# Optimization experiments

Hardware: AMD Instinct MI355X
Metric: run time of the kernel (lower is better)

## Reference

```python
import jax, jax.numpy as jnp
import numpy as np

N = 100000   # nodes
E = 3200000  # directed edges
EPS = 1e-5   # batchnorm eps


def setup_inputs() -> dict:
    key = jax.random.key(0)
    ks = jax.random.split(key, 12)
    x = jax.random.normal(ks[0], (N, 128), jnp.float32)
    edge_index = jax.random.randint(ks[1], (2, E), 0, N, dtype=jnp.int32).astype(jnp.int64)
    W1 = jax.random.normal(ks[2], (128, 256), jnp.float32) * (1.0 / np.sqrt(128))
    W2 = jax.random.normal(ks[3], (256, 256), jnp.float32) * (1.0 / np.sqrt(256))
    W3 = jax.random.normal(ks[4], (256, 40), jnp.float32) * (1.0 / np.sqrt(256))
    return {
        "x": x, "edge_index": edge_index,
        "W1": W1, "b1": jnp.zeros((256,), jnp.float32),
        "W2": W2, "b2": jnp.zeros((256,), jnp.float32),
        "W3": W3, "b3": jnp.zeros((40,), jnp.float32),
        "g1": jnp.ones((256,), jnp.float32), "be1": jnp.zeros((256,), jnp.float32),
        "g2": jnp.ones((256,), jnp.float32), "be2": jnp.zeros((256,), jnp.float32),
    }


def _gcn_conv(x, src, dst, norm, W, b):
    # GCNConv: transform then normalized sparse aggregation (A_hat @ (x W)) + b
    h = x @ W                              # [N, F_out]
    msg = h[src] * norm[:, None]           # gather + edge scaling, [E+N, F_out]
    return jax.ops.segment_sum(msg, dst, num_segments=N) + b


def _bn(h, g, b):
    # BatchNorm over the node dimension (batch stats, biased variance)
    m = h.mean(axis=0)
    v = h.var(axis=0)
    return (h - m) * jax.lax.rsqrt(v + EPS) * g + b


def reference(x, edge_index, W1, b1, W2, b2, W3, b3, g1, be1, g2, be2):
    # add self-loops (A + I), symmetric degree normalization D^-1/2 (A+I) D^-1/2
    loop = jnp.arange(N, dtype=edge_index.dtype)
    src = jnp.concatenate([edge_index[0], loop])
    dst = jnp.concatenate([edge_index[1], loop])
    deg = jax.ops.segment_sum(jnp.ones_like(src, jnp.float32), dst, num_segments=N)
    dinv = jax.lax.rsqrt(jnp.maximum(deg, 1.0))
    norm = dinv[src] * dinv[dst]           # [E+N]

    h = _gcn_conv(x, src, dst, norm, W1, b1)
    h = jax.nn.relu(_bn(h, g1, be1))       # dropout: identity (eval mode)
    h = _gcn_conv(h, src, dst, norm, W2, b2)
    h = jax.nn.relu(_bn(h, g2, be2))
    h = _gcn_conv(h, src, dst, norm, W3, b3)
    return jax.nn.log_softmax(h, axis=1)
```

## Files before the change

### kernel.cpp

```cpp
#include <hip/hip_runtime.h>
#include <hip/hip_bf16.h>
#include <math.h>

#define NNODES 100000
#define NEDGES 3200000
#define BN_EPS 1e-5f
#define NCH 391

typedef unsigned int uint;
typedef unsigned short ushort;
typedef __attribute__((ext_vector_type(8))) short bf16x8;
typedef __attribute__((ext_vector_type(4))) float f32x4;

__device__ inline float bflo(uint u) { return __uint_as_float(u << 16); }
__device__ inline float bfhi(uint u) { return __uint_as_float(u & 0xffff0000u); }
__device__ inline ushort f2bf(float f) {
    __hip_bfloat16 h = __float2bfloat16(f);
    union { __hip_bfloat16 b; ushort u; } c; c.b = h; return c.u;
}


__global__ void k_setup(const int* __restrict__ edst, int* __restrict__ cnt,
                        const float* __restrict__ x, ushort* __restrict__ xbf16,
                        const float* __restrict__ W1, const float* __restrict__ W2,
                        const float* __restrict__ W3, ushort* __restrict__ W1t,
                        ushort* __restrict__ W2t, ushort* __restrict__ W3t) {
    int b = blockIdx.x;
    if (b < 6250) {
        int e = (b * 256 + threadIdx.x) * 2;
        int2 v = *(const int2*)(edst + e);
        atomicAdd(&cnt[v.x], 1);
        atomicAdd(&cnt[v.y], 1);
    } else if (b < 18750) {
        int i = (b - 6250) * 256 + threadIdx.x;
        float4 v = ((const float4*)x)[i];
        ushort4 o; o.x=f2bf(v.x); o.y=f2bf(v.y); o.z=f2bf(v.z); o.w=f2bf(v.w);
        ((ushort4*)xbf16)[i] = o;
    } else {
        int bb = b - 18750;
        if (bb < 256) {
            for (int k = threadIdx.x; k < 128; k += 256)
                W1t[bb * 128 + k] = f2bf(W1[(size_t)k * 256 + bb]);
        } else if (bb < 512) {
            int n = bb - 256;
            for (int k = threadIdx.x; k < 256; k += 256)
                W2t[n * 256 + k] = f2bf(W2[(size_t)k * 256 + n]);
        } else {
            int n = bb - 512;
            for (int k = threadIdx.x; k < 256; k += 256)
                W3t[n * 256 + k] = (n < 40) ? f2bf(W3[(size_t)k * 40 + n]) : (ushort)0;
        }
    }
}

__global__ void k_deg(const int* __restrict__ cnt, float* __restrict__ dinv,
                      int* __restrict__ chunksums) {
    __shared__ int s[256];
    int i = blockIdx.x * 256 + threadIdx.x;
    int c = (i < NNODES) ? cnt[i] : 0;
    if (i < NNODES) dinv[i] = rsqrtf((float)c + 1.0f);
    s[threadIdx.x] = c;
    __syncthreads();
    for (int o = 128; o > 0; o >>= 1) {
        if (threadIdx.x < o) s[threadIdx.x] += s[threadIdx.x + o];
        __syncthreads();
    }
    if (threadIdx.x == 0) chunksums[blockIdx.x] = s[0];
}

__global__ void k_scan1(int* __restrict__ chunksums, int* __restrict__ rowstart) {
    __shared__ int s[512];
    int t = threadIdx.x;
    int v = (t < NCH) ? chunksums[t] : 0;
    s[t] = v;
    __syncthreads();
    for (int o = 1; o < 512; o <<= 1) {
        int add = (t >= o) ? s[t - o] : 0;
        __syncthreads();
        s[t] += add;
        __syncthreads();
    }
    if (t < NCH) chunksums[t] = s[t] - v;
    if (t == NCH - 1) rowstart[NNODES] = s[t];
}

__global__ void k_scan2(const int* __restrict__ cnt, const int* __restrict__ chunkbase,
                        int* __restrict__ rowstart, int* __restrict__ cursor) {
    __shared__ int s[256];
    int t = threadIdx.x;
    int i = blockIdx.x * 256 + t;
    int v = (i < NNODES) ? cnt[i] : 0;
    s[t] = v;
    __syncthreads();
    for (int o = 1; o < 256; o <<= 1) {
        int add = (t >= o) ? s[t - o] : 0;
        __syncthreads();
        s[t] += add;
        __syncthreads();
    }
    if (i < NNODES) {
        int excl = s[t] - v + chunkbase[blockIdx.x];
        rowstart[i] = excl;
        cursor[i]   = excl;
    }
}

__global__ void k_scatter(const int* __restrict__ src, const int* __restrict__ dst,
                          const float* __restrict__ dinv, int* __restrict__ cursor,
                          int2* __restrict__ pairs) {
    int e = blockIdx.x * 256 + threadIdx.x;
    if (e >= NEDGES) return;
    int s = src[e], d = dst[e];
    int p = atomicAdd(&cursor[d], 1);
    float w = dinv[s] * dinv[d];
    pairs[p] = make_int2(s, __float_as_int(w));
}


template <int F, int U>
__global__ __launch_bounds__(256) void k_aggh(
    const ushort* __restrict__ X, ushort* __restrict__ Y,
    const int2* __restrict__ pairs, const int* __restrict__ rowstart,
    const float* __restrict__ dinv) {
    constexpr int CPL = F / 32;
    const int wv = threadIdx.x >> 6;
    const int lane = threadIdx.x & 63;
    const int h = lane >> 5, l32 = lane & 31;
    const int d = blockIdx.x * 4 + wv;
    const int r0 = rowstart[d], r1 = rowstart[d + 1];
    const ushort* Xb = X + (size_t)CPL * l32;
    float acc[CPL] = {};
    int p = r0;
    for (; p + 2 * U <= r1; p += 2 * U) {
        int2 e[U];
#pragma unroll
        for (int j = 0; j < U; ++j) e[j] = pairs[p + 2 * j + h];
        if constexpr (CPL == 8) {
            uint4 u[U];
#pragma unroll
            for (int j = 0; j < U; ++j) u[j] = *(const uint4*)(Xb + (size_t)e[j].x * F);
#pragma unroll
            for (int j = 0; j < U; ++j) {
                float w = __int_as_float(e[j].y);
                acc[0]=fmaf(w,bflo(u[j].x),acc[0]); acc[1]=fmaf(w,bfhi(u[j].x),acc[1]);
                acc[2]=fmaf(w,bflo(u[j].y),acc[2]); acc[3]=fmaf(w,bfhi(u[j].y),acc[3]);
                acc[4]=fmaf(w,bflo(u[j].z),acc[4]); acc[5]=fmaf(w,bfhi(u[j].z),acc[5]);
                acc[6]=fmaf(w,bflo(u[j].w),acc[6]); acc[7]=fmaf(w,bfhi(u[j].w),acc[7]);
            }
        } else {
            uint2 u[U];
#pragma unroll
            for (int j = 0; j < U; ++j) u[j] = *(const uint2*)(Xb + (size_t)e[j].x * F);
#pragma unroll
            for (int j = 0; j < U; ++j) {
                float w = __int_as_float(e[j].y);
                acc[0]=fmaf(w,bflo(u[j].x),acc[0]); acc[1]=fmaf(w,bfhi(u[j].x),acc[1]);
                acc[2]=fmaf(w,bflo(u[j].y),acc[2]); acc[3]=fmaf(w,bfhi(u[j].y),acc[3]);
            }
        }
    }
    for (; p + 2 <= r1; p += 2) {
        int2 e = pairs[p + h];
        float w = __int_as_float(e.y);
        if constexpr (CPL == 8) {
            uint4 u = *(const uint4*)(Xb + (size_t)e.x * F);
            acc[0]=fmaf(w,bflo(u.x),acc[0]); acc[1]=fmaf(w,bfhi(u.x),acc[1]);
            acc[2]=fmaf(w,bflo(u.y),acc[2]); acc[3]=fmaf(w,bfhi(u.y),acc[3]);
            acc[4]=fmaf(w,bflo(u.z),acc[4]); acc[5]=fmaf(w,bfhi(u.z),acc[5]);
            acc[6]=fmaf(w,bflo(u.w),acc[6]); acc[7]=fmaf(w,bfhi(u.w),acc[7]);
        } else {
            uint2 u = *(const uint2*)(Xb + (size_t)e.x * F);
            acc[0]=fmaf(w,bflo(u.x),acc[0]); acc[1]=fmaf(w,bfhi(u.x),acc[1]);
            acc[2]=fmaf(w,bflo(u.y),acc[2]); acc[3]=fmaf(w,bfhi(u.y),acc[3]);
        }
    }
    if (p < r1 && h == 0) {
        int2 e = pairs[p];
        float w = __int_as_float(e.y);
        if constexpr (CPL == 8) {
            uint4 u = *(const uint4*)(Xb + (size_t)e.x * F);
            acc[0]=fmaf(w,bflo(u.x),acc[0]); acc[1]=fmaf(w,bfhi(u.x),acc[1]);
            acc[2]=fmaf(w,bflo(u.y),acc[2]); acc[3]=fmaf(w,bfhi(u.y),acc[3]);
            acc[4]=fmaf(w,bflo(u.z),acc[4]); acc[5]=fmaf(w,bfhi(u.z),acc[5]);
            acc[6]=fmaf(w,bflo(u.w),acc[6]); acc[7]=fmaf(w,bfhi(u.w),acc[7]);
        } else {
            uint2 u = *(const uint2*)(Xb + (size_t)e.x * F);
            acc[0]=fmaf(w,bflo(u.x),acc[0]); acc[1]=fmaf(w,bfhi(u.x),acc[1]);
            acc[2]=fmaf(w,bflo(u.y),acc[2]); acc[3]=fmaf(w,bfhi(u.y),acc[3]);
        }
    }
#pragma unroll
    for (int c = 0; c < CPL; ++c) acc[c] += __shfl_xor(acc[c], 32);
    if (h == 0) {
        float di = dinv[d], ws = di * di;
        if constexpr (CPL == 8) {
            uint4 u = *(const uint4*)(Xb + (size_t)d * F);
            acc[0]=fmaf(ws,bflo(u.x),acc[0]); acc[1]=fmaf(ws,bfhi(u.x),acc[1]);
            acc[2]=fmaf(ws,bflo(u.y),acc[2]); acc[3]=fmaf(ws,bfhi(u.y),acc[3]);
            acc[4]=fmaf(ws,bflo(u.z),acc[4]); acc[5]=fmaf(ws,bfhi(u.z),acc[5]);
            acc[6]=fmaf(ws,bflo(u.w),acc[6]); acc[7]=fmaf(ws,bfhi(u.w),acc[7]);
            uint4 o;
            o.x = (uint)f2bf(acc[0]) | ((uint)f2bf(acc[1]) << 16);
            o.y = (uint)f2bf(acc[2]) | ((uint)f2bf(acc[3]) << 16);
            o.z = (uint)f2bf(acc[4]) | ((uint)f2bf(acc[5]) << 16);
            o.w = (uint)f2bf(acc[6]) | ((uint)f2bf(acc[7]) << 16);
            *(uint4*)(Y + (size_t)d * F + CPL * l32) = o;
        } else {
            uint2 u = *(const uint2*)(Xb + (size_t)d * F);
            acc[0]=fmaf(ws,bflo(u.x),acc[0]); acc[1]=fmaf(ws,bfhi(u.x),acc[1]);
            acc[2]=fmaf(ws,bflo(u.y),acc[2]); acc[3]=fmaf(ws,bfhi(u.y),acc[3]);
            uint2 o;
            o.x = (uint)f2bf(acc[0]) | ((uint)f2bf(acc[1]) << 16);
            o.y = (uint)f2bf(acc[2]) | ((uint)f2bf(acc[3]) << 16);
            *(uint2*)(Y + (size_t)d * F + CPL * l32) = o;
        }
    }
}


__global__ __launch_bounds__(256) void k_agg40lsm(
    const ushort* __restrict__ X, float* __restrict__ out,
    const int2* __restrict__ pairs, const int* __restrict__ rowstart,
    const float* __restrict__ dinv, const float* __restrict__ bias) {
    int t = threadIdx.x;
    int wid = t >> 6, lane = t & 63;
    int sub = lane >> 5, l32 = lane & 31;
    int d = blockIdx.x * 8 + wid * 2 + sub;
    bool act = l32 < 20;
    int col = act ? 2 * l32 : 0;
    const int r0 = rowstart[d], r1 = rowstart[d + 1];
    float a0 = 0.f, a1 = 0.f;
    int p = r0;
    for (; p + 8 <= r1; p += 8) {
        int2 e[8]; uint u[8];
#pragma unroll
        for (int j = 0; j < 8; ++j) e[j] = pairs[p + j];
#pragma unroll
        for (int j = 0; j < 8; ++j) u[j] = *(const uint*)(X + (size_t)e[j].x * 40 + col);
#pragma unroll
        for (int j = 0; j < 8; ++j) {
            float w = __int_as_float(e[j].y);
            a0 = fmaf(w, bflo(u[j]), a0); a1 = fmaf(w, bfhi(u[j]), a1);
        }
    }
    for (; p < r1; ++p) {
        int2 e = pairs[p];
        uint u = *(const uint*)(X + (size_t)e.x * 40 + col);
        float w_ = __int_as_float(e.y);
        a0 = fmaf(w_, bflo(u), a0); a1 = fmaf(w_, bfhi(u), a1);
    }
    float di = dinv[d], ws = di * di;
    uint us = *(const uint*)(X + (size_t)d * 40 + col);
    a0 = fmaf(ws, bflo(us), a0); a1 = fmaf(ws, bfhi(us), a1);
    if (act) { a0 += bias[col]; a1 += bias[col + 1]; }
    else     { a0 = -INFINITY;  a1 = -INFINITY; }
    float mx = fmaxf(a0, a1);
    for (int o = 16; o > 0; o >>= 1) mx = fmaxf(mx, __shfl_xor(mx, o, 32));
    float e = act ? (expf(a0 - mx) + expf(a1 - mx)) : 0.f;
    float s = e;
    for (int o = 16; o > 0; o >>= 1) s += __shfl_xor(s, o, 32);
    float ls = logf(s);
    if (act)
        *(float2*)(out + (size_t)d * 40 + col) = make_float2(a0 - mx - ls, a1 - mx - ls);
}


__device__ inline bf16x8 bnrelu8(bf16x8 v, const float* scsh, int ch) {
    bf16x8 r;
#pragma unroll
    for (int j = 0; j < 8; ++j) {
        float f = __uint_as_float(((uint)(ushort)v[j]) << 16);
        f = fmaxf(fmaf(f, scsh[ch + j], scsh[256 + ch + j]), 0.f);
        r[j] = (short)f2bf(f);
    }
    return r;
}

template <int K, bool BNA, bool STATS>
__global__ __launch_bounds__(256) void k_gmm(
    const ushort* __restrict__ A, const ushort* __restrict__ Bt,
    const float* __restrict__ bsums, const float* __restrict__ g,
    const float* __restrict__ be, ushort* __restrict__ C,
    float* __restrict__ sums_out) {
    __shared__ ushort As[128 * 32];
    __shared__ ushort Bs[128 * 32];
    __shared__ float scsh[512];
    if constexpr (BNA) {
        int c = threadIdx.x;
        float mean = bsums[c] * (1.0f / NNODES);
        float var  = bsums[256 + c] * (1.0f / NNODES) - mean * mean;
        float sc = g[c] * rsqrtf(var + BN_EPS);
        scsh[c] = sc;
        scsh[256 + c] = be[c] - mean * sc;
        __syncthreads();
    }
    const int m0 = blockIdx.x * 128;
    const int n0 = blockIdx.y * 128;
    const int tid = threadIdx.x;
    const int lane = tid & 63;
    const int wid = tid >> 6;
    const int wr = wid >> 1, wc = wid & 1;
    const int sr1 = tid >> 2, sc_ = tid & 3;
    const int sr2 = sr1 + 64;
    const int ssl1 = sr1 * 32 + ((sc_ ^ ((sr1 >> 1) & 3)) * 8);
    const int ssl2 = sr2 * 32 + ((sc_ ^ ((sr2 >> 1) & 3)) * 8);
    const size_t ga1 = (size_t)min(m0 + sr1, NNODES - 1) * K + sc_ * 8;
    const size_t ga2 = (size_t)min(m0 + sr2, NNODES - 1) * K + sc_ * 8;
    const size_t gb1 = (size_t)(n0 + sr1) * K + sc_ * 8;
    const size_t gb2 = (size_t)(n0 + sr2) * K + sc_ * 8;
    const int kc = lane >> 4, rr = lane & 15;
    f32x4 acc[4][4] = {};
    for (int k0 = 0; k0 < K; k0 += 32) {
        bf16x8 av1 = *(const bf16x8*)(A + ga1 + k0);
        bf16x8 av2 = *(const bf16x8*)(A + ga2 + k0);
        bf16x8 bv1 = *(const bf16x8*)(Bt + gb1 + k0);
        bf16x8 bv2 = *(const bf16x8*)(Bt + gb2 + k0);
        if constexpr (BNA) {
            int ch = k0 + sc_ * 8;
            av1 = bnrelu8(av1, scsh, ch);
            av2 = bnrelu8(av2, scsh, ch);
        }
        if (k0) __syncthreads();
        *(bf16x8*)(As + ssl1) = av1;
        *(bf16x8*)(As + ssl2) = av2;
        *(bf16x8*)(Bs + ssl1) = bv1;
        *(bf16x8*)(Bs + ssl2) = bv2;
        __syncthreads();
        bf16x8 af[4], bfr[4];
#pragma unroll
        for (int f = 0; f < 4; ++f) {
            int ar = wr * 64 + f * 16 + rr;
            int br = wc * 64 + f * 16 + rr;
            af[f]  = *(const bf16x8*)(As + ar * 32 + ((kc ^ ((ar >> 1) & 3)) * 8));
            bfr[f] = *(const bf16x8*)(Bs + br * 32 + ((kc ^ ((br >> 1) & 3)) * 8));
        }
#pragma unroll
        for (int fm = 0; fm < 4; ++fm)
#pragma unroll
            for (int fn = 0; fn < 4; ++fn)
                acc[fm][fn] = __builtin_amdgcn_mfma_f32_16x16x32_bf16(af[fm], bfr[fn], acc[fm][fn], 0, 0, 0);
    }
    const int crow0 = m0 + wr * 64 + (lane >> 4) * 4;
    const int ccol0 = n0 + wc * 64 + (lane & 15);
#pragma unroll
    for (int fm = 0; fm < 4; ++fm) {
#pragma unroll
        for (int r = 0; r < 4; ++r) {
            int m = crow0 + fm * 16 + r;
            if (m >= NNODES) continue;
#pragma unroll
            for (int fn = 0; fn < 4; ++fn)
                C[(size_t)m * 256 + ccol0 + fn * 16] = f2bf(acc[fm][fn][r]);
        }
    }
    if constexpr (STATS) {
#pragma unroll
        for (int fn = 0; fn < 4; ++fn) {
            float s = 0.f, s2 = 0.f;
#pragma unroll
            for (int fm = 0; fm < 4; ++fm)
#pragma unroll
                for (int r = 0; r < 4; ++r) {
                    int m = crow0 + fm * 16 + r;
                    if (m < NNODES) { float v = acc[fm][fn][r]; s += v; s2 += v * v; }
                }
            s  += __shfl_xor(s, 16);  s  += __shfl_xor(s, 32);
            s2 += __shfl_xor(s2, 16); s2 += __shfl_xor(s2, 32);
            if (lane < 16) {
                int ch = ccol0 + fn * 16;
                atomicAdd(&sums_out[ch], s);
                atomicAdd(&sums_out[256 + ch], s2);
            }
        }
    }
}


__global__ __launch_bounds__(256) void k_gmm3m(
    const ushort* __restrict__ A, const ushort* __restrict__ Bt,
    const float* __restrict__ bsums, const float* __restrict__ g,
    const float* __restrict__ be, ushort* __restrict__ C) {
    __shared__ ushort As[128 * 64];
    __shared__ ushort Bs[48 * 64];
    __shared__ float scsh[512];
    {
        int c = threadIdx.x;
        float mean = bsums[c] * (1.0f / NNODES);
        float var  = bsums[256 + c] * (1.0f / NNODES) - mean * mean;
        float sc = g[c] * rsqrtf(var + BN_EPS);
        scsh[c] = sc;
        scsh[256 + c] = be[c] - mean * sc;
        __syncthreads();
    }
    const int m0 = blockIdx.x * 128;
    const int tid = threadIdx.x;
    const int lane = tid & 63;
    const int wm = tid >> 6;
    const int kc = lane >> 4, rr = lane & 15;
    f32x4 acc[2][3] = {};
    for (int k0 = 0; k0 < 256; k0 += 64) {
        bf16x8 avs[4];
        int arow[4], ach[4];
#pragma unroll
        for (int i = 0; i < 4; ++i) {
            int c = i * 256 + tid;
            arow[i] = c >> 3; ach[i] = c & 7;
            int m = min(m0 + arow[i], NNODES - 1);
            bf16x8 v = *(const bf16x8*)(A + (size_t)m * 256 + k0 + ach[i] * 8);
            avs[i] = bnrelu8(v, scsh, k0 + ach[i] * 8);
        }
        bf16x8 bvs[2];
#pragma unroll
        for (int i = 0; i < 2; ++i) {
            int c = i * 256 + tid;
            if (c < 384) {
                int row = c >> 3, ch = c & 7;
                bvs[i] = *(const bf16x8*)(Bt + (size_t)row * 256 + k0 + ch * 8);
            }
        }
        if (k0) __syncthreads();
#pragma unroll
        for (int i = 0; i < 4; ++i)
            *(bf16x8*)(As + arow[i] * 64 + ((ach[i] ^ (arow[i] & 7)) * 8)) = avs[i];
#pragma unroll
        for (int i = 0; i < 2; ++i) {
            int c = i * 256 + tid;
            if (c < 384) {
                int row = c >> 3, ch = c & 7;
                *(bf16x8*)(Bs + row * 64 + ((ch ^ (row & 7)) * 8)) = bvs[i];
            }
        }
        __syncthreads();
#pragma unroll
        for (int ks = 0; ks < 2; ++ks) {
            bf16x8 af[2], bfm[3];
#pragma unroll
            for (int fm = 0; fm < 2; ++fm) {
                int ar = wm * 32 + fm * 16 + rr;
                af[fm] = *(const bf16x8*)(As + ar * 64 + (((ks * 4 + kc) ^ (ar & 7)) * 8));
            }
#pragma unroll
            for (int fn = 0; fn < 3; ++fn) {
                int br = fn * 16 + rr;
                bfm[fn] = *(const bf16x8*)(Bs + br * 64 + (((ks * 4 + kc) ^ (br & 7)) * 8));
            }
#pragma unroll
            for (int fm = 0; fm < 2; ++fm)
#pragma unroll
                for (int fn = 0; fn < 3; ++fn)
                    acc[fm][fn] = __builtin_amdgcn_mfma_f32_16x16x32_bf16(af[fm], bfm[fn], acc[fm][fn], 0, 0, 0);
        }
    }
    const int crow0 = m0 + wm * 32 + (lane >> 4) * 4;
    const int ccol = lane & 15;
#pragma unroll
    for (int fm = 0; fm < 2; ++fm)
#pragma unroll
        for (int r = 0; r < 4; ++r) {
            int m = crow0 + fm * 16 + r;
            if (m >= NNODES) continue;
#pragma unroll
            for (int fn = 0; fn < 3; ++fn) {
                int col = fn * 16 + ccol;
                if (col < 40) C[(size_t)m * 40 + col] = f2bf(acc[fm][fn][r]);
            }
        }
}


__global__ void k_bnstats_bf(const uint* __restrict__ H, float* __restrict__ sums) {
    int t = threadIdx.x;
    int pp = t & 127, half = t >> 7;
    size_t row0 = (size_t)blockIdx.x * 256 + half * 128;
    float s0=0, s20=0, s1=0, s21=0;
    for (int i = 0; i < 128; ++i) {
        size_t m = row0 + i;
        if (m >= NNODES) break;
        uint u = H[m * 128 + pp];
        float v0 = bflo(u), v1 = bfhi(u);
        s0 += v0; s20 += v0*v0; s1 += v1; s21 += v1*v1;
    }
    atomicAdd(&sums[2*pp],       s0);
    atomicAdd(&sums[2*pp+1],     s1);
    atomicAdd(&sums[256+2*pp],   s20);
    atomicAdd(&sums[256+2*pp+1], s21);
}


extern "C" void kernel_launch(void* const* d_in, const int* in_sizes, int n_in,
                              void* d_out, int out_size, void* d_ws, size_t ws_size,
                              hipStream_t stream) {
    const float* x  = (const float*)d_in[0];
    const int*   ei = (const int*)d_in[1];
    const float* W1 = (const float*)d_in[2];
    const float* W2 = (const float*)d_in[4];
    const float* W3 = (const float*)d_in[6];
    const float* b3 = (const float*)d_in[7];
    const float* g1 = (const float*)d_in[8];
    const float* be1 = (const float*)d_in[9];
    const float* g2 = (const float*)d_in[10];
    const float* be2 = (const float*)d_in[11];
    float* out = (float*)d_out;

    const int* esrc = ei;
    const int* edst = ei + NEDGES;

    char* p = (char*)d_ws;
    auto alloc = [&](size_t bytes) { char* r = p; p += (bytes + 511) & ~(size_t)511; return r; };
    float* dinv     = (float*)alloc((size_t)NNODES * 4);
    int*   cnt      = (int*)  alloc((size_t)NNODES * 4);
    int*   rowstart = (int*)  alloc((size_t)(NNODES + 1) * 4);
    int*   cursor   = (int*)  alloc((size_t)NNODES * 4);
    int*   chunksums= (int*)  alloc((size_t)NCH * 4);
    float* stats    = (float*)alloc((size_t)2048 * 4);
    ushort* W1t     = (ushort*)alloc((size_t)256 * 128 * 2);
    ushort* W2t     = (ushort*)alloc((size_t)256 * 256 * 2);
    ushort* W3t     = (ushort*)alloc((size_t)48 * 256 * 2);
    int2*  pairs    = (int2*) alloc((size_t)NEDGES * 8);
    char*  R1       = alloc((size_t)NNODES * 256 * 2);
    char*  R2       = alloc((size_t)NNODES * 256 * 2);
    char*  R3       = alloc((size_t)NNODES * 256 * 2);

    ushort* xbf16 = (ushort*)R1;
    ushort* P_bf  = (ushort*)R1 + (size_t)NNODES * 128;
    ushort* t3_bf = (ushort*)R1;
    ushort* h1_bf = (ushort*)R2;
    ushort* h2_bf = (ushort*)R2;
    ushort* t_bf  = (ushort*)R3;

    float* sums1 = stats;
    float* sums2 = stats + 1024;

    hipMemsetAsync(cnt, 0, (size_t)NNODES * 4, stream);
    hipMemsetAsync(stats, 0, (size_t)2048 * 4, stream);

    k_setup<<<19310, 256, 0, stream>>>(edst, cnt, x, xbf16, W1, W2, W3, W1t, W2t, W3t);
    k_deg<<<NCH, 256, 0, stream>>>(cnt, dinv, chunksums);
    k_scan1<<<1, 512, 0, stream>>>(chunksums, rowstart);
    k_scan2<<<NCH, 256, 0, stream>>>(cnt, chunksums, rowstart, cursor);
    k_scatter<<<NEDGES / 256, 256, 0, stream>>>(esrc, edst, dinv, cursor, pairs);

    dim3 ggrid((NNODES + 127) / 128, 2);

    k_aggh<128, 8><<<NNODES / 4, 256, 0, stream>>>(xbf16, P_bf, pairs, rowstart, dinv);
    k_gmm<128, false, true><<<ggrid, 256, 0, stream>>>(P_bf, W1t, nullptr, nullptr, nullptr, h1_bf, sums1);

    k_gmm<256, true, false><<<ggrid, 256, 0, stream>>>(h1_bf, W2t, sums1, g1, be1, t_bf, nullptr);
    k_aggh<256, 8><<<NNODES / 4, 256, 0, stream>>>(t_bf, h2_bf, pairs, rowstart, dinv);
    k_bnstats_bf<<<NCH, 256, 0, stream>>>((const uint*)h2_bf, sums2);

    k_gmm3m<<<(NNODES + 127) / 128, 256, 0, stream>>>(h2_bf, W3t, sums2, g2, be2, t3_bf);
    k_agg40lsm<<<NNODES / 8, 256, 0, stream>>>(t3_bf, out, pairs, rowstart, dinv, b3);
}
```

Measured before the change: 906.8 us.

## Store only source indices in CSR and recompute edge weights from dinv

```diff
diff --git a/kernel.cpp b/kernel.cpp
--- a/kernel.cpp
+++ b/kernel.cpp
@@ -106,21 +106,19 @@
 }
 
 __global__ void k_scatter(const int* __restrict__ src, const int* __restrict__ dst,
-                          const float* __restrict__ dinv, int* __restrict__ cursor,
-                          int2* __restrict__ pairs) {
-    int e = blockIdx.x * 256 + threadIdx.x;
-    if (e >= NEDGES) return;
-    int s = src[e], d = dst[e];
-    int p = atomicAdd(&cursor[d], 1);
-    float w = dinv[s] * dinv[d];
-    pairs[p] = make_int2(s, __float_as_int(w));
+                          int* __restrict__ cursor, int* __restrict__ pairs) {
+    int e = (blockIdx.x * 256 + threadIdx.x) * 2;
+    int2 ss = *(const int2*)(src + e);
+    int2 dd = *(const int2*)(dst + e);
+    int p0 = atomicAdd(&cursor[dd.x], 1); pairs[p0] = ss.x;
+    int p1 = atomicAdd(&cursor[dd.y], 1); pairs[p1] = ss.y;
 }
 
 
 template <int F, int U>
 __global__ __launch_bounds__(256) void k_aggh(
     const ushort* __restrict__ X, ushort* __restrict__ Y,
-    const int2* __restrict__ pairs, const int* __restrict__ rowstart,
+    const int* __restrict__ pairs, const int* __restrict__ rowstart,
     const float* __restrict__ dinv) {
     constexpr int CPL = F / 32;
     const int wv = threadIdx.x >> 6;
@@ -128,20 +126,23 @@
     const int h = lane >> 5, l32 = lane & 31;
     const int d = blockIdx.x * 4 + wv;
     const int r0 = rowstart[d], r1 = rowstart[d + 1];
+    const float dinv_d = dinv[d];
     const ushort* Xb = X + (size_t)CPL * l32;
     float acc[CPL] = {};
     int p = r0;
     for (; p + 2 * U <= r1; p += 2 * U) {
-        int2 e[U];
+        int e[U]; float wv_[U];
 #pragma unroll
         for (int j = 0; j < U; ++j) e[j] = pairs[p + 2 * j + h];
         if constexpr (CPL == 8) {
             uint4 u[U];
 #pragma unroll
-            for (int j = 0; j < U; ++j) u[j] = *(const uint4*)(Xb + (size_t)e[j].x * F);
+            for (int j = 0; j < U; ++j) u[j] = *(const uint4*)(Xb + (size_t)e[j] * F);
+#pragma unroll
+            for (int j = 0; j < U; ++j) wv_[j] = dinv[e[j]];
 #pragma unroll
             for (int j = 0; j < U; ++j) {
-                float w = __int_as_float(e[j].y);
+                float w = dinv_d * wv_[j];
                 acc[0]=fmaf(w,bflo(u[j].x),acc[0]); acc[1]=fmaf(w,bfhi(u[j].x),acc[1]);
                 acc[2]=fmaf(w,bflo(u[j].y),acc[2]); acc[3]=fmaf(w,bfhi(u[j].y),acc[3]);
                 acc[4]=fmaf(w,bflo(u[j].z),acc[4]); acc[5]=fmaf(w,bfhi(u[j].z),acc[5]);
@@ -150,41 +151,43 @@
         } else {
             uint2 u[U];
 #pragma unroll
-            for (int j = 0; j < U; ++j) u[j] = *(const uint2*)(Xb + (size_t)e[j].x * F);
+            for (int j = 0; j < U; ++j) u[j] = *(const uint2*)(Xb + (size_t)e[j] * F);
+#pragma unroll
+            for (int j = 0; j < U; ++j) wv_[j] = dinv[e[j]];
 #pragma unroll
             for (int j = 0; j < U; ++j) {
-                float w = __int_as_float(e[j].y);
+                float w = dinv_d * wv_[j];
                 acc[0]=fmaf(w,bflo(u[j].x),acc[0]); acc[1]=fmaf(w,bfhi(u[j].x),acc[1]);
                 acc[2]=fmaf(w,bflo(u[j].y),acc[2]); acc[3]=fmaf(w,bfhi(u[j].y),acc[3]);
             }
         }
     }
     for (; p + 2 <= r1; p += 2) {
-        int2 e = pairs[p + h];
-        float w = __int_as_float(e.y);
+        int e = pairs[p + h];
+        float w = dinv_d * dinv[e];
         if constexpr (CPL == 8) {
-            uint4 u = *(const uint4*)(Xb + (size_t)e.x * F);
+            uint4 u = *(const uint4*)(Xb + (size_t)e * F);
             acc[0]=fmaf(w,bflo(u.x),acc[0]); acc[1]=fmaf(w,bfhi(u.x),acc[1]);
             acc[2]=fmaf(w,bflo(u.y),acc[2]); acc[3]=fmaf(w,bfhi(u.y),acc[3]);
             acc[4]=fmaf(w,bflo(u.z),acc[4]); acc[5]=fmaf(w,bfhi(u.z),acc[5]);
             acc[6]=fmaf(w,bflo(u.w),acc[6]); acc[7]=fmaf(w,bfhi(u.w),acc[7]);
         } else {
-            uint2 u = *(const uint2*)(Xb + (size_t)e.x * F);
+            uint2 u = *(const uint2*)(Xb + (size_t)e * F);
             acc[0]=fmaf(w,bflo(u.x),acc[0]); acc[1]=fmaf(w,bfhi(u.x),acc[1]);
             acc[2]=fmaf(w,bflo(u.y),acc[2]); acc[3]=fmaf(w,bfhi(u.y),acc[3]);
         }
     }
     if (p < r1 && h == 0) {
-        int2 e = pairs[p];
-        float w = __int_as_float(e.y);
+        int e = pairs[p];
+        float w = dinv_d * dinv[e];
         if constexpr (CPL == 8) {
-            uint4 u = *(const uint4*)(Xb + (size_t)e.x * F);
+            uint4 u = *(const uint4*)(Xb + (size_t)e * F);
             acc[0]=fmaf(w,bflo(u.x),acc[0]); acc[1]=fmaf(w,bfhi(u.x),acc[1]);
             acc[2]=fmaf(w,bflo(u.y),acc[2]); acc[3]=fmaf(w,bfhi(u.y),acc[3]);
             acc[4]=fmaf(w,bflo(u.z),acc[4]); acc[5]=fmaf(w,bfhi(u.z),acc[5]);
             acc[6]=fmaf(w,bflo(u.w),acc[6]); acc[7]=fmaf(w,bfhi(u.w),acc[7]);
         } else {
-            uint2 u = *(const uint2*)(Xb + (size_t)e.x * F);
+            uint2 u = *(const uint2*)(Xb + (size_t)e * F);
             acc[0]=fmaf(w,bflo(u.x),acc[0]); acc[1]=fmaf(w,bfhi(u.x),acc[1]);
             acc[2]=fmaf(w,bflo(u.y),acc[2]); acc[3]=fmaf(w,bfhi(u.y),acc[3]);
         }
@@ -192,7 +195,7 @@
 #pragma unroll
     for (int c = 0; c < CPL; ++c) acc[c] += __shfl_xor(acc[c], 32);
     if (h == 0) {
-        float di = dinv[d], ws = di * di;
+        float ws = dinv_d * dinv_d;
         if constexpr (CPL == 8) {
             uint4 u = *(const uint4*)(Xb + (size_t)d * F);
             acc[0]=fmaf(ws,bflo(u.x),acc[0]); acc[1]=fmaf(ws,bfhi(u.x),acc[1]);
@@ -220,7 +223,7 @@
 
 __global__ __launch_bounds__(256) void k_agg40lsm(
     const ushort* __restrict__ X, float* __restrict__ out,
-    const int2* __restrict__ pairs, const int* __restrict__ rowstart,
+    const int* __restrict__ pairs, const int* __restrict__ rowstart,
     const float* __restrict__ dinv, const float* __restrict__ bias) {
     int t = threadIdx.x;
     int wid = t >> 6, lane = t & 63;
@@ -229,28 +232,31 @@
     bool act = l32 < 20;
     int col = act ? 2 * l32 : 0;
     const int r0 = rowstart[d], r1 = rowstart[d + 1];
+    const float dinv_d = dinv[d];
     float a0 = 0.f, a1 = 0.f;
     int p = r0;
     for (; p + 8 <= r1; p += 8) {
-        int2 e[8]; uint u[8];
+        int e[8]; uint u[8]; float wv[8];
 #pragma unroll
         for (int j = 0; j < 8; ++j) e[j] = pairs[p + j];
 #pragma unroll
-        for (int j = 0; j < 8; ++j) u[j] = *(const uint*)(X + (size_t)e[j].x * 40 + col);
+        for (int j = 0; j < 8; ++j) u[j] = *(const uint*)(X + (size_t)e[j] * 64 + col);
+#pragma unroll
+        for (int j = 0; j < 8; ++j) wv[j] = dinv[e[j]];
 #pragma unroll
         for (int j = 0; j < 8; ++j) {
-            float w = __int_as_float(e[j].y);
+            float w = dinv_d * wv[j];
             a0 = fmaf(w, bflo(u[j]), a0); a1 = fmaf(w, bfhi(u[j]), a1);
         }
     }
     for (; p < r1; ++p) {
-        int2 e = pairs[p];
-        uint u = *(const uint*)(X + (size_t)e.x * 40 + col);
-        float w_ = __int_as_float(e.y);
+        int e = pairs[p];
+        uint u = *(const uint*)(X + (size_t)e * 64 + col);
+        float w_ = dinv_d * dinv[e];
         a0 = fmaf(w_, bflo(u), a0); a1 = fmaf(w_, bfhi(u), a1);
     }
-    float di = dinv[d], ws = di * di;
-    uint us = *(const uint*)(X + (size_t)d * 40 + col);
+    float ws = dinv_d * dinv_d;
+    uint us = *(const uint*)(X + (size_t)d * 64 + col);
     a0 = fmaf(ws, bflo(us), a0); a1 = fmaf(ws, bfhi(us), a1);
     if (act) { a0 += bias[col]; a1 += bias[col + 1]; }
     else     { a0 = -INFINITY;  a1 = -INFINITY; }
@@ -462,7 +468,7 @@
 #pragma unroll
             for (int fn = 0; fn < 3; ++fn) {
                 int col = fn * 16 + ccol;
-                if (col < 40) C[(size_t)m * 40 + col] = f2bf(acc[fm][fn][r]);
+                if (col < 40) C[(size_t)m * 64 + col] = f2bf(acc[fm][fn][r]);
             }
         }
 }
@@ -516,7 +522,7 @@
     ushort* W1t     = (ushort*)alloc((size_t)256 * 128 * 2);
     ushort* W2t     = (ushort*)alloc((size_t)256 * 256 * 2);
     ushort* W3t     = (ushort*)alloc((size_t)48 * 256 * 2);
-    int2*  pairs    = (int2*) alloc((size_t)NEDGES * 8);
+    int*   pairs    = (int*)  alloc((size_t)NEDGES * 4);
     char*  R1       = alloc((size_t)NNODES * 256 * 2);
     char*  R2       = alloc((size_t)NNODES * 256 * 2);
     char*  R3       = alloc((size_t)NNODES * 256 * 2);
@@ -538,7 +544,7 @@
     k_deg<<<NCH, 256, 0, stream>>>(cnt, dinv, chunksums);
     k_scan1<<<1, 512, 0, stream>>>(chunksums, rowstart);
     k_scan2<<<NCH, 256, 0, stream>>>(cnt, chunksums, rowstart, cursor);
-    k_scatter<<<NEDGES / 256, 256, 0, stream>>>(esrc, edst, dinv, cursor, pairs);
+    k_scatter<<<NEDGES / 512, 256, 0, stream>>>(esrc, edst, cursor, pairs);
 
     dim3 ggrid((NNODES + 127) / 128, 2);
 
```

Measured after the change: 999.0 us. 10.2% more time.
